# Kernel tuning notes

Hardware: AMD Instinct MI355X
Metric: run time of the kernel (lower is better)

## Reference

```python
import jax, jax.numpy as jnp
import numpy as np

N = 100000      # nodes
E = 1600000     # edges
R = 16          # relation types
IN_DIM = 32
HID = 64
NCLS = 8
B = 128         # graphs in batch


def setup_inputs() -> dict:
    key = jax.random.key(0)
    ks = jax.random.split(key, 16)
    h = jax.random.normal(ks[0], (N, IN_DIM), dtype=jnp.float32)
    src = jax.random.randint(ks[1], (E,), 0, N, dtype=jnp.int32)
    dst = jax.random.randint(ks[2], (E,), 0, N, dtype=jnp.int32)
    rel_types = jax.random.randint(ks[3], (E,), 0, R, dtype=jnp.int32)
    node2graph = jnp.sort(jax.random.randint(ks[4], (N,), 0, B, dtype=jnp.int32))
    s1 = 1.0 / np.sqrt(IN_DIM)
    s2 = 1.0 / np.sqrt(HID)
    W1 = jax.random.normal(ks[5], (R, IN_DIM, HID), dtype=jnp.float32) * s1
    Wloop1 = jax.random.normal(ks[6], (IN_DIM, HID), dtype=jnp.float32) * s1
    b1 = jnp.zeros((HID,), dtype=jnp.float32)
    W2 = jax.random.normal(ks[7], (R, HID, HID), dtype=jnp.float32) * s2
    Wloop2 = jax.random.normal(ks[8], (HID, HID), dtype=jnp.float32) * s2
    b2 = jnp.zeros((HID,), dtype=jnp.float32)
    Wc = jax.random.normal(ks[9], (HID, NCLS), dtype=jnp.float32) * s2
    bc = jnp.zeros((NCLS,), dtype=jnp.float32)
    return {"h": h, "src": src, "dst": dst, "rel_types": rel_types,
            "node2graph": node2graph, "W1": W1, "Wloop1": Wloop1, "b1": b1,
            "W2": W2, "Wloop2": Wloop2, "b2": b2, "Wc": Wc, "bc": bc}


def rel_graph_conv(h, src, dst, rel, W, Wloop, b):
    # h: [N, in], W: [R, in, out]. Transform all nodes by all relations once
    # (R small), then gather per-edge message indexed by (rel, src) and
    # scatter-sum to dst -- same math as DGL RelGraphConv (no edge norm),
    # with self-loop and bias (DGL defaults self_loop=True, bias=True).
    HR = jnp.einsum('ni,rio->rno', h, W)          # [R, N, out]
    msg = HR[rel, src]                            # [E, out]
    agg = jax.ops.segment_sum(msg, dst, num_segments=h.shape[0])
    return agg + h @ Wloop + b


def reference(h, src, dst, rel_types, node2graph,
              W1, Wloop1, b1, W2, Wloop2, b2, Wc, bc):
    h = h.astype(jnp.float32)
    h = jax.nn.relu(rel_graph_conv(h, src, dst, rel_types, W1, Wloop1, b1))
    h = jax.nn.relu(rel_graph_conv(h, src, dst, rel_types, W2, Wloop2, b2))
    # dgl.mean_nodes: per-graph mean pooling over nodes
    sums = jax.ops.segment_sum(h, node2graph, num_segments=B)      # [B, HID]
    cnts = jax.ops.segment_sum(jnp.ones((h.shape[0],), jnp.float32),
                               node2graph, num_segments=B)
    hg = sums / jnp.maximum(cnts, 1.0)[:, None]
    logits = hg @ Wc + bc
    return jax.nn.softmax(logits, axis=1)
```

## Files before the change

kernel.cpp:

```cpp
#include <hip/hip_runtime.h>
#include <hip/hip_bf16.h>


#define IN_DIM 32
#define HID 64
#define NREL 16
#define NCLS 8

__device__ __forceinline__ int rfl(int v) { return __builtin_amdgcn_readfirstlane(v); }


__global__ void hist_rel(const int* __restrict__ rel, int* __restrict__ hist, int E) {
  __shared__ int lh[NREL];
  int tid = threadIdx.x;
  if (tid < NREL) lh[tid] = 0;
  __syncthreads();
  for (int e = blockIdx.x * blockDim.x + tid; e < E; e += gridDim.x * blockDim.x)
    atomicAdd(&lh[rel[e]], 1);
  __syncthreads();
  if (tid < NREL && lh[tid] > 0) atomicAdd(&hist[tid], lh[tid]);
}

__global__ void scan16(const int* __restrict__ hist, int* __restrict__ offs,
                       int* __restrict__ fill) {
  if (threadIdx.x == 0) {
    int o = 0;
    for (int r = 0; r < NREL; ++r) {
      offs[r] = o;
      fill[r] = o;
      o += (hist[r] + 63) & ~63;
    }
    offs[NREL] = o;
  }
}

__global__ void fill_pad(int* __restrict__ ssrc, int* __restrict__ sdst, int Epad, int N) {
  int i = blockIdx.x * blockDim.x + threadIdx.x;
  if (i < Epad) { ssrc[i] = 0; sdst[i] = N; }
}

__global__ void scatter_rel(const int* __restrict__ rel, const int* __restrict__ src,
                            const int* __restrict__ dst, int* __restrict__ fill,
                            int* __restrict__ ssrc, int* __restrict__ sdst, int E) {
  __shared__ int lc[NREL];
  __shared__ int lbase[NREL];
  int tid = threadIdx.x;
  if (tid < NREL) lc[tid] = 0;
  __syncthreads();
  int e = blockIdx.x * blockDim.x + tid;
  int r = 0, lo = 0;
  bool valid = (e < E);
  if (valid) {
    r = rel[e];
    lo = atomicAdd(&lc[r], 1);
  }
  __syncthreads();
  if (tid < NREL && lc[tid] > 0) lbase[tid] = atomicAdd(&fill[tid], lc[tid]);
  __syncthreads();
  if (valid) {
    int p = lbase[r] + lo;
    ssrc[p] = src[e];
    sdst[p] = dst[e];
  }
}


template <int IN>
__global__ void edge_layer(const float* __restrict__ hin,
                           const int* __restrict__ ssrc,
                           const int* __restrict__ sdst,
                           const float* __restrict__ W,
                           const int* __restrict__ offs,
                           float* __restrict__ agg,
                           int maxchunks) {
  const int lane = threadIdx.x & 63;
  int wid = rfl((int)(blockIdx.x * (blockDim.x >> 6) + (threadIdx.x >> 6)));
  if (wid >= maxchunks) return;
  const int base = wid * 64;

  int r = 0;
#pragma unroll
  for (int k = 1; k < NREL; ++k) r += (base >= offs[k]) ? 1 : 0;

  const float* Wr = W + (size_t)r * (IN * HID);
  float w[IN];
#pragma unroll
  for (int i = 0; i < IN; ++i) w[i] = Wr[i * HID + lane];

  const int myd = sdst[base + lane];
  const int mys = ssrc[base + lane];

#pragma unroll 4
  for (int k = 0; k < 64; ++k) {
    const int d = __builtin_amdgcn_readlane(myd, k);
    const int s = __builtin_amdgcn_readlane(mys, k);
    const float4* __restrict__ row = (const float4*)(hin + (size_t)s * IN);
    float a0 = 0.f, a1 = 0.f, a2 = 0.f, a3 = 0.f;
#pragma unroll
    for (int i = 0; i < IN / 4; ++i) {
      float4 hv = row[i];
      a0 = fmaf(hv.x, w[4 * i + 0], a0);
      a1 = fmaf(hv.y, w[4 * i + 1], a1);
      a2 = fmaf(hv.z, w[4 * i + 2], a2);
      a3 = fmaf(hv.w, w[4 * i + 3], a3);
    }
    atomicAdd(&agg[(size_t)d * HID + lane], (a0 + a1) + (a2 + a3));
  }
}


__global__ void finalize1(const float* __restrict__ agg, const float* __restrict__ h,
                          const float* __restrict__ Wl, const float* __restrict__ b,
                          float* __restrict__ h1, int N) {
  const int lane = threadIdx.x & 63;
  int wid = rfl((int)(blockIdx.x * (blockDim.x >> 6) + (threadIdx.x >> 6)));
  int nw = gridDim.x * (blockDim.x >> 6);
  float wl[IN_DIM];
#pragma unroll
  for (int i = 0; i < IN_DIM; ++i) wl[i] = Wl[i * HID + lane];
  float bv = b[lane];
  for (int n = wid; n < N; n += nw) {
    const float4* __restrict__ row = (const float4*)(h + (size_t)n * IN_DIM);
    float a0 = 0.f, a1 = 0.f, a2 = 0.f, a3 = 0.f;
#pragma unroll
    for (int i = 0; i < IN_DIM / 4; ++i) {
      float4 hv = row[i];
      a0 = fmaf(hv.x, wl[4 * i + 0], a0);
      a1 = fmaf(hv.y, wl[4 * i + 1], a1);
      a2 = fmaf(hv.z, wl[4 * i + 2], a2);
      a3 = fmaf(hv.w, wl[4 * i + 3], a3);
    }
    float v = agg[(size_t)n * HID + lane] + (a0 + a1) + (a2 + a3) + bv;
    h1[(size_t)n * HID + lane] = fmaxf(v, 0.f);
  }
}

__global__ void finalize2_pool(const float* __restrict__ agg, const float* __restrict__ h1,
                               const float* __restrict__ Wl, const float* __restrict__ b,
                               const int* __restrict__ n2g,
                               float* __restrict__ pooled, float* __restrict__ cnt, int N) {
  const int lane = threadIdx.x & 63;
  int wid = rfl((int)(blockIdx.x * (blockDim.x >> 6) + (threadIdx.x >> 6)));
  int nw = gridDim.x * (blockDim.x >> 6);
  int per = (N + nw - 1) / nw;
  int n0 = wid * per;
  int n1 = min(N, n0 + per);
  if (n0 >= n1) return;

  float wl[HID];
#pragma unroll
  for (int i = 0; i < HID; ++i) wl[i] = Wl[i * HID + lane];
  float bv = b[lane];

  float psum = 0.f, pcnt = 0.f;
  int pg = -1;
  for (int n = n0; n < n1; ++n) {
    const float4* __restrict__ row = (const float4*)(h1 + (size_t)n * HID);
    float a0 = 0.f, a1 = 0.f, a2 = 0.f, a3 = 0.f;
#pragma unroll
    for (int i = 0; i < HID / 4; ++i) {
      float4 hv = row[i];
      a0 = fmaf(hv.x, wl[4 * i + 0], a0);
      a1 = fmaf(hv.y, wl[4 * i + 1], a1);
      a2 = fmaf(hv.z, wl[4 * i + 2], a2);
      a3 = fmaf(hv.w, wl[4 * i + 3], a3);
    }
    float v = agg[(size_t)n * HID + lane] + (a0 + a1) + (a2 + a3) + bv;
    v = fmaxf(v, 0.f);
    int g = rfl(n2g[n]);
    if (g != pg) {
      if (pg >= 0) {
        atomicAdd(&pooled[(size_t)pg * HID + lane], psum);
        if (lane == 0) atomicAdd(&cnt[pg], pcnt);
      }
      pg = g; psum = 0.f; pcnt = 0.f;
    }
    psum += v; pcnt += 1.f;
  }
  if (pg >= 0) {
    atomicAdd(&pooled[(size_t)pg * HID + lane], psum);
    if (lane == 0) atomicAdd(&cnt[pg], pcnt);
  }
}


__global__ void classifier(const float* __restrict__ pooled, const float* __restrict__ cnt,
                           const float* __restrict__ Wc, const float* __restrict__ bc,
                           float* __restrict__ out, int B) {
  int g = blockIdx.x * blockDim.x + threadIdx.x;
  if (g >= B) return;
  float c = fmaxf(cnt[g], 1.f);
  float lg[NCLS];
#pragma unroll
  for (int cc = 0; cc < NCLS; ++cc) lg[cc] = bc[cc];
  for (int k = 0; k < HID; ++k) {
    float hg = pooled[(size_t)g * HID + k] / c;
#pragma unroll
    for (int cc = 0; cc < NCLS; ++cc) lg[cc] = fmaf(hg, Wc[k * NCLS + cc], lg[cc]);
  }
  float m = lg[0];
#pragma unroll
  for (int cc = 1; cc < NCLS; ++cc) m = fmaxf(m, lg[cc]);
  float s = 0.f;
#pragma unroll
  for (int cc = 0; cc < NCLS; ++cc) { lg[cc] = __expf(lg[cc] - m); s += lg[cc]; }
  float inv = 1.f / s;
#pragma unroll
  for (int cc = 0; cc < NCLS; ++cc) out[(size_t)g * NCLS + cc] = lg[cc] * inv;
}


extern "C" void kernel_launch(void* const* d_in, const int* in_sizes, int n_in,
                              void* d_out, int out_size, void* d_ws, size_t ws_size,
                              hipStream_t stream) {
  const float* h   = (const float*)d_in[0];
  const int* src   = (const int*)d_in[1];
  const int* dst   = (const int*)d_in[2];
  const int* rel   = (const int*)d_in[3];
  const int* n2g   = (const int*)d_in[4];
  const float* W1  = (const float*)d_in[5];
  const float* Wl1 = (const float*)d_in[6];
  const float* b1  = (const float*)d_in[7];
  const float* W2  = (const float*)d_in[8];
  const float* Wl2 = (const float*)d_in[9];
  const float* b2  = (const float*)d_in[10];
  const float* Wc  = (const float*)d_in[11];
  const float* bc  = (const float*)d_in[12];

  const int N = in_sizes[0] / IN_DIM;
  const int E = in_sizes[1];
  const int B = out_size / NCLS;

  const int maxchunks = (E + 63) / 64 + NREL;
  const int Epad = maxchunks * 64;

  float* agg    = (float*)d_ws;
  float* h1     = agg + (size_t)(N + 1) * HID;
  int*   ssrc   = (int*)(h1 + (size_t)N * HID);
  int*   sdst   = ssrc + Epad;
  int*   hist   = sdst + Epad;
  int*   offs   = hist + NREL;
  int*   fill   = offs + NREL + 1;
  float* pooled = (float*)(fill + NREL);
  float* cnt    = pooled + (size_t)B * HID;

  hipMemsetAsync(hist, 0, NREL * sizeof(int), stream);
  hipMemsetAsync(pooled, 0, (size_t)(B * HID + B) * sizeof(float), stream);

  fill_pad<<<(Epad + 255) / 256, 256, 0, stream>>>(ssrc, sdst, Epad, N);
  hist_rel<<<1024, 256, 0, stream>>>(rel, hist, E);
  scan16<<<1, 64, 0, stream>>>(hist, offs, fill);
  scatter_rel<<<(E + 255) / 256, 256, 0, stream>>>(rel, src, dst, fill, ssrc, sdst, E);

  const int eblocks = (maxchunks + 3) / 4;

  hipMemsetAsync(agg, 0, (size_t)(N + 1) * HID * sizeof(float), stream);
  edge_layer<IN_DIM><<<eblocks, 256, 0, stream>>>(h, ssrc, sdst, W1, offs, agg, maxchunks);
  finalize1<<<2048, 256, 0, stream>>>(agg, h, Wl1, b1, h1, N);

  hipMemsetAsync(agg, 0, (size_t)(N + 1) * HID * sizeof(float), stream);
  edge_layer<HID><<<eblocks, 256, 0, stream>>>(h1, ssrc, sdst, W2, offs, agg, maxchunks);
  finalize2_pool<<<2048, 256, 0, stream>>>(agg, h1, Wl2, b2, n2g, pooled, cnt, N);

  classifier<<<(B + 127) / 128, 128, 0, stream>>>(pooled, cnt, Wc, bc, (float*)d_out, B);
}
```

Measured before the change: 980.0 us.

## Replace atomic scatter-add with per-edge message buffer and CSR gather by destination

Builds a destination CSR (histogram, three-stage scan, and an edge index into the relation-sorted order), then writes per-edge messages to a dense buffer and has each node gather its incoming messages. The self-loop, bias, ReLU and pooling are fused into the gather. This removes the float atomics on agg and its memsets. In exchange it writes and rereads a roughly 400 MB message buffer per layer and adds several preprocessing kernels. The new path runs only when the workspace is large enough, otherwise the old path is kept.

```diff
diff --git a/kernel.cpp b/kernel.cpp
--- a/kernel.cpp
+++ b/kernel.cpp
@@ -6,8 +6,10 @@
 #define HID 64
 #define NREL 16
 #define NCLS 8
+#define CHUNK 2048
 
 __device__ __forceinline__ int rfl(int v) { return __builtin_amdgcn_readfirstlane(v); }
+__device__ __forceinline__ int rl(int v, int l) { return __builtin_amdgcn_readlane(v, l); }
 
 
 __global__ void hist_rel(const int* __restrict__ rel, int* __restrict__ hist, int E) {
@@ -21,18 +23,241 @@
   if (tid < NREL && lh[tid] > 0) atomicAdd(&hist[tid], lh[tid]);
 }
 
+__global__ void hist_dst_k(const int* __restrict__ dst, int* __restrict__ histd, int E) {
+  for (int e = blockIdx.x * blockDim.x + threadIdx.x; e < E; e += gridDim.x * blockDim.x)
+    atomicAdd(&histd[dst[e]], 1);
+}
+
 __global__ void scan16(const int* __restrict__ hist, int* __restrict__ offs,
-                       int* __restrict__ fill) {
+                       int* __restrict__ fillrel) {
   if (threadIdx.x == 0) {
     int o = 0;
     for (int r = 0; r < NREL; ++r) {
       offs[r] = o;
-      fill[r] = o;
+      fillrel[r] = o;
       o += (hist[r] + 63) & ~63;
     }
     offs[NREL] = o;
   }
 }
+
+__global__ void pad_gaps(const int* __restrict__ hist, const int* __restrict__ offs,
+                         int* __restrict__ ssrc, int Epad) {
+  int r = blockIdx.x;
+  int lo = (r < NREL) ? offs[r] + hist[r] : offs[NREL];
+  int hi = (r < NREL) ? offs[r + 1] : Epad;
+  for (int i = lo + threadIdx.x; i < hi; i += blockDim.x) ssrc[i] = 0;
+}
+
+
+__global__ void scan1_k(const int* __restrict__ histd, int* __restrict__ csum, int N) {
+  __shared__ int red[256];
+  int t = threadIdx.x;
+  int base = blockIdx.x * CHUNK + t * 8;
+  int s = 0;
+#pragma unroll
+  for (int i = 0; i < 8; ++i) { int idx = base + i; s += (idx < N) ? histd[idx] : 0; }
+  red[t] = s; __syncthreads();
+  for (int off = 128; off > 0; off >>= 1) {
+    if (t < off) red[t] += red[t + off];
+    __syncthreads();
+  }
+  if (t == 0) csum[blockIdx.x] = red[0];
+}
+
+__global__ void scan2_k(const int* __restrict__ csum, int* __restrict__ cbase,
+                        int* __restrict__ rowptr, int nchunks, int N) {
+  if (threadIdx.x == 0) {
+    int run = 0;
+    for (int c = 0; c < nchunks; ++c) { cbase[c] = run; run += csum[c]; }
+    rowptr[N] = run;
+  }
+}
+
+__global__ void scan3_k(const int* __restrict__ histd, const int* __restrict__ cbase,
+                        int* __restrict__ rowptr, int* __restrict__ filldst, int N) {
+  __shared__ int ts[256];
+  int t = threadIdx.x;
+  int base = blockIdx.x * CHUNK + t * 8;
+  int v[8]; int s = 0;
+#pragma unroll
+  for (int i = 0; i < 8; ++i) { int idx = base + i; int x = (idx < N) ? histd[idx] : 0; v[i] = x; s += x; }
+  ts[t] = s; __syncthreads();
+  int x = s;
+  for (int off = 1; off < 256; off <<= 1) {
+    int y = (t >= off) ? ts[t - off] : 0;
+    __syncthreads();
+    x += y; ts[t] = x;
+    __syncthreads();
+  }
+  int run = cbase[blockIdx.x] + x - s;
+#pragma unroll
+  for (int i = 0; i < 8; ++i) {
+    int idx = base + i;
+    if (idx < N) { rowptr[idx] = run; filldst[idx] = run; run += v[i]; }
+  }
+}
+
+
+__global__ void scatter_rel2(const int* __restrict__ rel, const int* __restrict__ src,
+                             const int* __restrict__ dst, int* __restrict__ fillrel,
+                             int* __restrict__ filldst, int* __restrict__ ssrc,
+                             int* __restrict__ eidx, int E) {
+  __shared__ int lc[NREL];
+  __shared__ int lbase[NREL];
+  int tid = threadIdx.x;
+  if (tid < NREL) lc[tid] = 0;
+  __syncthreads();
+  int e = blockIdx.x * blockDim.x + tid;
+  int r = 0, lo = 0;
+  bool valid = (e < E);
+  if (valid) { r = rel[e]; lo = atomicAdd(&lc[r], 1); }
+  __syncthreads();
+  if (tid < NREL && lc[tid] > 0) lbase[tid] = atomicAdd(&fillrel[tid], lc[tid]);
+  __syncthreads();
+  if (valid) {
+    int p = lbase[r] + lo;
+    ssrc[p] = src[e];
+    int q = atomicAdd(&filldst[dst[e]], 1);
+    eidx[q] = p;
+  }
+}
+
+
+template <int IN>
+__global__ void edge_msg(const float* __restrict__ hin, const int* __restrict__ ssrc,
+                         const float* __restrict__ W, const int* __restrict__ offs,
+                         float* __restrict__ msg, int maxchunks) {
+  const int lane = threadIdx.x & 63;
+  int wid = rfl((int)(blockIdx.x * (blockDim.x >> 6) + (threadIdx.x >> 6)));
+  if (wid >= maxchunks) return;
+  const int base = wid * 64;
+
+  int r = 0;
+#pragma unroll
+  for (int k = 1; k < NREL; ++k) r += (base >= offs[k]) ? 1 : 0;
+
+  const float* Wr = W + (size_t)r * (IN * HID);
+  float w[IN];
+#pragma unroll
+  for (int i = 0; i < IN; ++i) w[i] = Wr[i * HID + lane];
+
+  const int mys = ssrc[base + lane];
+
+#pragma unroll 4
+  for (int k = 0; k < 64; ++k) {
+    const int s = rl(mys, k);
+    const float4* __restrict__ row = (const float4*)(hin + (size_t)s * IN);
+    float a0 = 0.f, a1 = 0.f, a2 = 0.f, a3 = 0.f;
+#pragma unroll
+    for (int i = 0; i < IN / 4; ++i) {
+      float4 hv = row[i];
+      a0 = fmaf(hv.x, w[4 * i + 0], a0);
+      a1 = fmaf(hv.y, w[4 * i + 1], a1);
+      a2 = fmaf(hv.z, w[4 * i + 2], a2);
+      a3 = fmaf(hv.w, w[4 * i + 3], a3);
+    }
+    msg[(size_t)(base + k) * HID + lane] = (a0 + a1) + (a2 + a3);
+  }
+}
+
+
+template <int IN, bool POOL>
+__global__ void gather_fin(const float* __restrict__ msg, const int* __restrict__ eidx,
+                           const int* __restrict__ rowptr, const float* __restrict__ hprev,
+                           const float* __restrict__ Wl, const float* __restrict__ b,
+                           const int* __restrict__ n2g, float* __restrict__ out,
+                           float* __restrict__ pooled, float* __restrict__ cnt, int N) {
+  const int lane = threadIdx.x & 63;
+  int wid = rfl((int)(blockIdx.x * (blockDim.x >> 6) + (threadIdx.x >> 6)));
+  int nw = gridDim.x * (blockDim.x >> 6);
+  int per = (N + nw - 1) / nw;
+  int n0 = wid * per, n1 = min(N, n0 + per);
+  if (n0 >= n1) return;
+
+  float wl[IN];
+#pragma unroll
+  for (int i = 0; i < IN; ++i) wl[i] = Wl[i * HID + lane];
+  float bv = b[lane];
+
+  float psum = 0.f, pcnt = 0.f;
+  int pg = -1;
+  for (int n = n0; n < n1; ++n) {
+    int j0 = rowptr[n], j1 = rowptr[n + 1];
+    float a0 = 0.f, a1 = 0.f, a2 = 0.f, a3 = 0.f;
+    int j = j0;
+    while (j < j1) {
+      int c = min(j1 - j, 64);
+      int vidx = (lane < c) ? eidx[j + lane] : 0;
+      int k = 0;
+      for (; k + 3 < c; k += 4) {
+        int i0 = rl(vidx, k), i1 = rl(vidx, k + 1), i2 = rl(vidx, k + 2), i3 = rl(vidx, k + 3);
+        a0 += msg[(size_t)i0 * HID + lane];
+        a1 += msg[(size_t)i1 * HID + lane];
+        a2 += msg[(size_t)i2 * HID + lane];
+        a3 += msg[(size_t)i3 * HID + lane];
+      }
+      for (; k < c; ++k) a0 += msg[(size_t)rl(vidx, k) * HID + lane];
+      j += c;
+    }
+    const float4* __restrict__ row = (const float4*)(hprev + (size_t)n * IN);
+    float s0 = 0.f, s1 = 0.f, s2 = 0.f, s3 = 0.f;
+#pragma unroll
+    for (int i = 0; i < IN / 4; ++i) {
+      float4 hv = row[i];
+      s0 = fmaf(hv.x, wl[4 * i + 0], s0);
+      s1 = fmaf(hv.y, wl[4 * i + 1], s1);
+      s2 = fmaf(hv.z, wl[4 * i + 2], s2);
+      s3 = fmaf(hv.w, wl[4 * i + 3], s3);
+    }
+    float v = (a0 + a1) + (a2 + a3) + (s0 + s1) + (s2 + s3) + bv;
+    v = fmaxf(v, 0.f);
+    if (POOL) {
+      int g = rfl(n2g[n]);
+      if (g != pg) {
+        if (pg >= 0) {
+          atomicAdd(&pooled[(size_t)pg * HID + lane], psum);
+          if (lane == 0) atomicAdd(&cnt[pg], pcnt);
+        }
+        pg = g; psum = 0.f; pcnt = 0.f;
+      }
+      psum += v; pcnt += 1.f;
+    } else {
+      out[(size_t)n * HID + lane] = v;
+    }
+  }
+  if (POOL && pg >= 0) {
+    atomicAdd(&pooled[(size_t)pg * HID + lane], psum);
+    if (lane == 0) atomicAdd(&cnt[pg], pcnt);
+  }
+}
+
+
+__global__ void classifier(const float* __restrict__ pooled, const float* __restrict__ cnt,
+                           const float* __restrict__ Wc, const float* __restrict__ bc,
+                           float* __restrict__ out, int B) {
+  int g = blockIdx.x * blockDim.x + threadIdx.x;
+  if (g >= B) return;
+  float c = fmaxf(cnt[g], 1.f);
+  float lg[NCLS];
+#pragma unroll
+  for (int cc = 0; cc < NCLS; ++cc) lg[cc] = bc[cc];
+  for (int k = 0; k < HID; ++k) {
+    float hg = pooled[(size_t)g * HID + k] / c;
+#pragma unroll
+    for (int cc = 0; cc < NCLS; ++cc) lg[cc] = fmaf(hg, Wc[k * NCLS + cc], lg[cc]);
+  }
+  float m = lg[0];
+#pragma unroll
+  for (int cc = 1; cc < NCLS; ++cc) m = fmaxf(m, lg[cc]);
+  float s = 0.f;
+#pragma unroll
+  for (int cc = 0; cc < NCLS; ++cc) { lg[cc] = __expf(lg[cc] - m); s += lg[cc]; }
+  float inv = 1.f / s;
+#pragma unroll
+  for (int cc = 0; cc < NCLS; ++cc) out[(size_t)g * NCLS + cc] = lg[cc] * inv;
+}
+
 
 __global__ void fill_pad(int* __restrict__ ssrc, int* __restrict__ sdst, int Epad, int N) {
   int i = blockIdx.x * blockDim.x + threadIdx.x;
@@ -50,50 +275,35 @@
   int e = blockIdx.x * blockDim.x + tid;
   int r = 0, lo = 0;
   bool valid = (e < E);
-  if (valid) {
-    r = rel[e];
-    lo = atomicAdd(&lc[r], 1);
-  }
+  if (valid) { r = rel[e]; lo = atomicAdd(&lc[r], 1); }
   __syncthreads();
   if (tid < NREL && lc[tid] > 0) lbase[tid] = atomicAdd(&fill[tid], lc[tid]);
   __syncthreads();
-  if (valid) {
-    int p = lbase[r] + lo;
-    ssrc[p] = src[e];
-    sdst[p] = dst[e];
-  }
-}
-
+  if (valid) { int p = lbase[r] + lo; ssrc[p] = src[e]; sdst[p] = dst[e]; }
+}
 
 template <int IN>
-__global__ void edge_layer(const float* __restrict__ hin,
-                           const int* __restrict__ ssrc,
-                           const int* __restrict__ sdst,
-                           const float* __restrict__ W,
-                           const int* __restrict__ offs,
-                           float* __restrict__ agg,
+__global__ void edge_layer(const float* __restrict__ hin, const int* __restrict__ ssrc,
+                           const int* __restrict__ sdst, const float* __restrict__ W,
+                           const int* __restrict__ offs, float* __restrict__ agg,
                            int maxchunks) {
   const int lane = threadIdx.x & 63;
   int wid = rfl((int)(blockIdx.x * (blockDim.x >> 6) + (threadIdx.x >> 6)));
   if (wid >= maxchunks) return;
   const int base = wid * 64;
-
   int r = 0;
 #pragma unroll
   for (int k = 1; k < NREL; ++k) r += (base >= offs[k]) ? 1 : 0;
-
   const float* Wr = W + (size_t)r * (IN * HID);
   float w[IN];
 #pragma unroll
   for (int i = 0; i < IN; ++i) w[i] = Wr[i * HID + lane];
-
   const int myd = sdst[base + lane];
   const int mys = ssrc[base + lane];
-
 #pragma unroll 4
   for (int k = 0; k < 64; ++k) {
-    const int d = __builtin_amdgcn_readlane(myd, k);
-    const int s = __builtin_amdgcn_readlane(mys, k);
+    const int d = rl(myd, k);
+    const int s = rl(mys, k);
     const float4* __restrict__ row = (const float4*)(hin + (size_t)s * IN);
     float a0 = 0.f, a1 = 0.f, a2 = 0.f, a3 = 0.f;
 #pragma unroll
@@ -107,7 +317,6 @@
     atomicAdd(&agg[(size_t)d * HID + lane], (a0 + a1) + (a2 + a3));
   }
 }
-
 
 __global__ void finalize1(const float* __restrict__ agg, const float* __restrict__ h,
                           const float* __restrict__ Wl, const float* __restrict__ b,
@@ -143,15 +352,12 @@
   int wid = rfl((int)(blockIdx.x * (blockDim.x >> 6) + (threadIdx.x >> 6)));
   int nw = gridDim.x * (blockDim.x >> 6);
   int per = (N + nw - 1) / nw;
-  int n0 = wid * per;
-  int n1 = min(N, n0 + per);
+  int n0 = wid * per, n1 = min(N, n0 + per);
   if (n0 >= n1) return;
-
   float wl[HID];
 #pragma unroll
   for (int i = 0; i < HID; ++i) wl[i] = Wl[i * HID + lane];
   float bv = b[lane];
-
   float psum = 0.f, pcnt = 0.f;
   int pg = -1;
   for (int n = n0; n < n1; ++n) {
@@ -181,32 +387,6 @@
     atomicAdd(&pooled[(size_t)pg * HID + lane], psum);
     if (lane == 0) atomicAdd(&cnt[pg], pcnt);
   }
-}
-
-
-__global__ void classifier(const float* __restrict__ pooled, const float* __restrict__ cnt,
-                           const float* __restrict__ Wc, const float* __restrict__ bc,
-                           float* __restrict__ out, int B) {
-  int g = blockIdx.x * blockDim.x + threadIdx.x;
-  if (g >= B) return;
-  float c = fmaxf(cnt[g], 1.f);
-  float lg[NCLS];
-#pragma unroll
-  for (int cc = 0; cc < NCLS; ++cc) lg[cc] = bc[cc];
-  for (int k = 0; k < HID; ++k) {
-    float hg = pooled[(size_t)g * HID + k] / c;
-#pragma unroll
-    for (int cc = 0; cc < NCLS; ++cc) lg[cc] = fmaf(hg, Wc[k * NCLS + cc], lg[cc]);
-  }
-  float m = lg[0];
-#pragma unroll
-  for (int cc = 1; cc < NCLS; ++cc) m = fmaxf(m, lg[cc]);
-  float s = 0.f;
-#pragma unroll
-  for (int cc = 0; cc < NCLS; ++cc) { lg[cc] = __expf(lg[cc] - m); s += lg[cc]; }
-  float inv = 1.f / s;
-#pragma unroll
-  for (int cc = 0; cc < NCLS; ++cc) out[(size_t)g * NCLS + cc] = lg[cc] * inv;
 }
 
 
@@ -233,6 +413,51 @@
 
   const int maxchunks = (E + 63) / 64 + NREL;
   const int Epad = maxchunks * 64;
+  const int nchunks = (N + CHUNK - 1) / CHUNK;
+  const int eblocks = (maxchunks + 3) / 4;
+
+  size_t need_elems = (size_t)N * HID + (size_t)Epad * HID + (size_t)Epad * 2 +
+                      (size_t)(N + 1) + N + N + nchunks * 2 + 49 +
+                      (size_t)B * HID + B + 64;
+  if (ws_size >= need_elems * 4) {
+    float* h1     = (float*)d_ws;
+    float* msg    = h1 + (size_t)N * HID;
+    int*   ssrc   = (int*)(msg + (size_t)Epad * HID);
+    int*   eidx   = ssrc + Epad;
+    int*   rowptr = eidx + Epad;
+    int*   filldst= rowptr + (N + 1);
+    int*   histd  = filldst + N;
+    int*   csum   = histd + N;
+    int*   cbase  = csum + nchunks;
+    int*   hist   = cbase + nchunks;
+    int*   offs   = hist + NREL;
+    int*   fillrel= offs + NREL + 1;
+    float* pooled = (float*)(fillrel + NREL);
+    float* cnt    = pooled + (size_t)B * HID;
+
+    hipMemsetAsync(hist, 0, NREL * sizeof(int), stream);
+    hipMemsetAsync(histd, 0, (size_t)N * sizeof(int), stream);
+    hipMemsetAsync(pooled, 0, (size_t)(B * HID + B) * sizeof(float), stream);
+
+    hist_rel<<<1024, 256, 0, stream>>>(rel, hist, E);
+    hist_dst_k<<<1024, 256, 0, stream>>>(dst, histd, E);
+    scan16<<<1, 64, 0, stream>>>(hist, offs, fillrel);
+    scan1_k<<<nchunks, 256, 0, stream>>>(histd, csum, N);
+    scan2_k<<<1, 64, 0, stream>>>(csum, cbase, rowptr, nchunks, N);
+    scan3_k<<<nchunks, 256, 0, stream>>>(histd, cbase, rowptr, filldst, N);
+    pad_gaps<<<NREL + 1, 64, 0, stream>>>(hist, offs, ssrc, Epad);
+    scatter_rel2<<<(E + 255) / 256, 256, 0, stream>>>(rel, src, dst, fillrel, filldst,
+                                                      ssrc, eidx, E);
+
+    edge_msg<IN_DIM><<<eblocks, 256, 0, stream>>>(h, ssrc, W1, offs, msg, maxchunks);
+    gather_fin<IN_DIM, false><<<1024, 256, 0, stream>>>(msg, eidx, rowptr, h, Wl1, b1,
+                                                        nullptr, h1, nullptr, nullptr, N);
+    edge_msg<HID><<<eblocks, 256, 0, stream>>>(h1, ssrc, W2, offs, msg, maxchunks);
+    gather_fin<HID, true><<<1024, 256, 0, stream>>>(msg, eidx, rowptr, h1, Wl2, b2,
+                                                    n2g, nullptr, pooled, cnt, N);
+    classifier<<<(B + 127) / 128, 128, 0, stream>>>(pooled, cnt, Wc, bc, (float*)d_out, B);
+    return;
+  }
 
   float* agg    = (float*)d_ws;
   float* h1     = agg + (size_t)(N + 1) * HID;
@@ -246,21 +471,15 @@
 
   hipMemsetAsync(hist, 0, NREL * sizeof(int), stream);
   hipMemsetAsync(pooled, 0, (size_t)(B * HID + B) * sizeof(float), stream);
-
   fill_pad<<<(Epad + 255) / 256, 256, 0, stream>>>(ssrc, sdst, Epad, N);
   hist_rel<<<1024, 256, 0, stream>>>(rel, hist, E);
   scan16<<<1, 64, 0, stream>>>(hist, offs, fill);
   scatter_rel<<<(E + 255) / 256, 256, 0, stream>>>(rel, src, dst, fill, ssrc, sdst, E);
-
-  const int eblocks = (maxchunks + 3) / 4;
-
   hipMemsetAsync(agg, 0, (size_t)(N + 1) * HID * sizeof(float), stream);
   edge_layer<IN_DIM><<<eblocks, 256, 0, stream>>>(h, ssrc, sdst, W1, offs, agg, maxchunks);
   finalize1<<<2048, 256, 0, stream>>>(agg, h, Wl1, b1, h1, N);
-
   hipMemsetAsync(agg, 0, (size_t)(N + 1) * HID * sizeof(float), stream);
   edge_layer<HID><<<eblocks, 256, 0, stream>>>(h1, ssrc, sdst, W2, offs, agg, maxchunks);
   finalize2_pool<<<2048, 256, 0, stream>>>(agg, h1, Wl2, b2, n2g, pooled, cnt, N);
-
   classifier<<<(B + 127) / 128, 128, 0, stream>>>(pooled, cnt, Wc, bc, (float*)d_out, B);
 }
```

Result: no change. 980.7 us (+0.1%).

## Replace relation-sorted atomic scatter with dst-sorted CSR gather and LDS-staged weights

Applied to the files above, without the earlier changes.

Builds a CSR by destination (histogram, three-stage scan, atomic fill) with src and relation packed into one int per edge. Each wave then owns a range of destination nodes and accumulates messages in registers, so the global float atomics of the edge pass go away. Relation weights are staged in swizzled shared memory in groups of relations, with one pass per group. The cost is re-reading the adjacency for every group (2 passes for layer 1, 4 for layer 2), a serial ballot loop per edge, and a CSR build that itself uses atomics. The old path is kept as a fallback when the workspace is too small.

```diff
diff --git a/kernel.cpp b/kernel.cpp
--- a/kernel.cpp
+++ b/kernel.cpp
@@ -6,105 +6,131 @@
 #define HID 64
 #define NREL 16
 #define NCLS 8
+#define CHUNK 2048
 
 __device__ __forceinline__ int rfl(int v) { return __builtin_amdgcn_readfirstlane(v); }
-
-
-__global__ void hist_rel(const int* __restrict__ rel, int* __restrict__ hist, int E) {
-  __shared__ int lh[NREL];
-  int tid = threadIdx.x;
-  if (tid < NREL) lh[tid] = 0;
-  __syncthreads();
-  for (int e = blockIdx.x * blockDim.x + tid; e < E; e += gridDim.x * blockDim.x)
-    atomicAdd(&lh[rel[e]], 1);
-  __syncthreads();
-  if (tid < NREL && lh[tid] > 0) atomicAdd(&hist[tid], lh[tid]);
-}
-
-__global__ void scan16(const int* __restrict__ hist, int* __restrict__ offs,
-                       int* __restrict__ fill) {
+__device__ __forceinline__ int rl(int v, int l) { return __builtin_amdgcn_readlane(v, l); }
+
+
+__global__ void hist_dst_k(const int* __restrict__ dst, int* __restrict__ histd, int E) {
+  for (int e = blockIdx.x * blockDim.x + threadIdx.x; e < E; e += gridDim.x * blockDim.x)
+    atomicAdd(&histd[dst[e]], 1);
+}
+
+__global__ void scan1_k(const int* __restrict__ histd, int* __restrict__ csum, int N) {
+  __shared__ int red[256];
+  int t = threadIdx.x;
+  int base = blockIdx.x * CHUNK + t * 8;
+  int s = 0;
+#pragma unroll
+  for (int i = 0; i < 8; ++i) { int idx = base + i; s += (idx < N) ? histd[idx] : 0; }
+  red[t] = s; __syncthreads();
+  for (int off = 128; off > 0; off >>= 1) {
+    if (t < off) red[t] += red[t + off];
+    __syncthreads();
+  }
+  if (t == 0) csum[blockIdx.x] = red[0];
+}
+
+__global__ void scan2_k(const int* __restrict__ csum, int* __restrict__ cbase,
+                        int* __restrict__ rowptr, int nchunks, int N) {
   if (threadIdx.x == 0) {
-    int o = 0;
-    for (int r = 0; r < NREL; ++r) {
-      offs[r] = o;
-      fill[r] = o;
-      o += (hist[r] + 63) & ~63;
-    }
-    offs[NREL] = o;
-  }
-}
-
-__global__ void fill_pad(int* __restrict__ ssrc, int* __restrict__ sdst, int Epad, int N) {
-  int i = blockIdx.x * blockDim.x + threadIdx.x;
-  if (i < Epad) { ssrc[i] = 0; sdst[i] = N; }
-}
-
-__global__ void scatter_rel(const int* __restrict__ rel, const int* __restrict__ src,
-                            const int* __restrict__ dst, int* __restrict__ fill,
-                            int* __restrict__ ssrc, int* __restrict__ sdst, int E) {
-  __shared__ int lc[NREL];
-  __shared__ int lbase[NREL];
-  int tid = threadIdx.x;
-  if (tid < NREL) lc[tid] = 0;
-  __syncthreads();
-  int e = blockIdx.x * blockDim.x + tid;
-  int r = 0, lo = 0;
-  bool valid = (e < E);
-  if (valid) {
-    r = rel[e];
-    lo = atomicAdd(&lc[r], 1);
-  }
-  __syncthreads();
-  if (tid < NREL && lc[tid] > 0) lbase[tid] = atomicAdd(&fill[tid], lc[tid]);
-  __syncthreads();
-  if (valid) {
-    int p = lbase[r] + lo;
-    ssrc[p] = src[e];
-    sdst[p] = dst[e];
-  }
-}
-
-
-template <int IN>
-__global__ void edge_layer(const float* __restrict__ hin,
-                           const int* __restrict__ ssrc,
-                           const int* __restrict__ sdst,
-                           const float* __restrict__ W,
-                           const int* __restrict__ offs,
-                           float* __restrict__ agg,
-                           int maxchunks) {
+    int run = 0;
+    for (int c = 0; c < nchunks; ++c) { cbase[c] = run; run += csum[c]; }
+    rowptr[N] = run;
+  }
+}
+
+__global__ void scan3_k(const int* __restrict__ histd, const int* __restrict__ cbase,
+                        int* __restrict__ rowptr, int* __restrict__ filldst, int N) {
+  __shared__ int ts[256];
+  int t = threadIdx.x;
+  int base = blockIdx.x * CHUNK + t * 8;
+  int v[8]; int s = 0;
+#pragma unroll
+  for (int i = 0; i < 8; ++i) { int idx = base + i; int x = (idx < N) ? histd[idx] : 0; v[i] = x; s += x; }
+  ts[t] = s; __syncthreads();
+  int x = s;
+  for (int off = 1; off < 256; off <<= 1) {
+    int y = (t >= off) ? ts[t - off] : 0;
+    __syncthreads();
+    x += y; ts[t] = x;
+    __syncthreads();
+  }
+  int run = cbase[blockIdx.x] + x - s;
+#pragma unroll
+  for (int i = 0; i < 8; ++i) {
+    int idx = base + i;
+    if (idx < N) { rowptr[idx] = run; filldst[idx] = run; run += v[i]; }
+  }
+}
+
+__global__ void scatter_pack(const int* __restrict__ src, const int* __restrict__ dst,
+                             const int* __restrict__ rel, int* __restrict__ filldst,
+                             int* __restrict__ epack, int E) {
+  int e = blockIdx.x * blockDim.x + threadIdx.x;
+  if (e < E) {
+    int q = atomicAdd(&filldst[dst[e]], 1);
+    epack[q] = (src[e] << 4) | rel[e];
+  }
+}
+
+
+template <int K, int GSZ, bool FIRST>
+__global__ __launch_bounds__(512, 4)
+void edge_pass(const float* __restrict__ hin, const int* __restrict__ epack,
+               const int* __restrict__ rowptr, const float* __restrict__ W,
+               float* __restrict__ out, int N, int g) {
+  __shared__ float lw[GSZ * K * 64];
+  const float* __restrict__ Wg = W + (size_t)g * GSZ * K * 64;
+  for (int s = threadIdx.x; s < GSZ * K * 64; s += blockDim.x) {
+    int rloc = s / (K * 64);
+    int rem  = s - rloc * (K * 64);
+    int i = rem >> 6;
+    int o = rem & 63;
+    lw[rloc * (K * 64) + o * K + ((o & (K - 1)) ^ i)] = Wg[s];
+  }
+  __syncthreads();
+
   const int lane = threadIdx.x & 63;
-  int wid = rfl((int)(blockIdx.x * (blockDim.x >> 6) + (threadIdx.x >> 6)));
-  if (wid >= maxchunks) return;
-  const int base = wid * 64;
-
-  int r = 0;
-#pragma unroll
-  for (int k = 1; k < NREL; ++k) r += (base >= offs[k]) ? 1 : 0;
-
-  const float* Wr = W + (size_t)r * (IN * HID);
-  float w[IN];
-#pragma unroll
-  for (int i = 0; i < IN; ++i) w[i] = Wr[i * HID + lane];
-
-  const int myd = sdst[base + lane];
-  const int mys = ssrc[base + lane];
-
-#pragma unroll 4
-  for (int k = 0; k < 64; ++k) {
-    const int d = __builtin_amdgcn_readlane(myd, k);
-    const int s = __builtin_amdgcn_readlane(mys, k);
-    const float4* __restrict__ row = (const float4*)(hin + (size_t)s * IN);
-    float a0 = 0.f, a1 = 0.f, a2 = 0.f, a3 = 0.f;
-#pragma unroll
-    for (int i = 0; i < IN / 4; ++i) {
-      float4 hv = row[i];
-      a0 = fmaf(hv.x, w[4 * i + 0], a0);
-      a1 = fmaf(hv.y, w[4 * i + 1], a1);
-      a2 = fmaf(hv.z, w[4 * i + 2], a2);
-      a3 = fmaf(hv.w, w[4 * i + 3], a3);
-    }
-    atomicAdd(&agg[(size_t)d * HID + lane], (a0 + a1) + (a2 + a3));
+  const int nw  = gridDim.x * (blockDim.x >> 6);
+  const int wid = blockIdx.x * (blockDim.x >> 6) + (threadIdx.x >> 6);
+  const int per = (N + nw - 1) / nw;
+  const int n0 = wid * per, n1 = min(N, n0 + per);
+  const int fb0 = lane * K + (lane & (K - 1));
+  const int SH = (GSZ == 8) ? 3 : 2;
+
+  for (int n = n0; n < n1; ++n) {
+    const int j0 = rowptr[n], j1 = rowptr[n + 1];
+    float acc = 0.f;
+    bool any = false;
+    for (int j = j0; j < j1; j += 64) {
+      const int c = min(j1 - j, 64);
+      const int bv = (lane < c) ? epack[j + lane] : 0;
+      unsigned long long m = __ballot(lane < c && (((bv & 15) >> SH) == g));
+      any |= (m != 0ull);
+      while (m) {
+        const int k = (int)__builtin_ctzll(m);
+        m &= m - 1;
+        const int v = rl(bv, k);
+        const int s = v >> 4;
+        const int rloc = (v & 15) - g * GSZ;
+        const float4* __restrict__ row = (const float4*)(hin + (size_t)s * K);
+        const float* __restrict__ lwp = lw + rloc * (K * 64);
+        float a0 = 0.f, a1 = 0.f, a2 = 0.f, a3 = 0.f;
+#pragma unroll
+        for (int q = 0; q < K / 4; ++q) {
+          float4 hv = row[q];
+          a0 = fmaf(hv.x, lwp[fb0 ^ (4 * q + 0)], a0);
+          a1 = fmaf(hv.y, lwp[fb0 ^ (4 * q + 1)], a1);
+          a2 = fmaf(hv.z, lwp[fb0 ^ (4 * q + 2)], a2);
+          a3 = fmaf(hv.w, lwp[fb0 ^ (4 * q + 3)], a3);
+        }
+        acc += (a0 + a1) + (a2 + a3);
+      }
+    }
+    if (FIRST) out[(size_t)n * HID + lane] = acc;
+    else if (any) out[(size_t)n * HID + lane] += acc;
   }
 }
 
@@ -143,15 +169,12 @@
   int wid = rfl((int)(blockIdx.x * (blockDim.x >> 6) + (threadIdx.x >> 6)));
   int nw = gridDim.x * (blockDim.x >> 6);
   int per = (N + nw - 1) / nw;
-  int n0 = wid * per;
-  int n1 = min(N, n0 + per);
+  int n0 = wid * per, n1 = min(N, n0 + per);
   if (n0 >= n1) return;
-
   float wl[HID];
 #pragma unroll
   for (int i = 0; i < HID; ++i) wl[i] = Wl[i * HID + lane];
   float bv = b[lane];
-
   float psum = 0.f, pcnt = 0.f;
   int pg = -1;
   for (int n = n0; n < n1; ++n) {
@@ -207,6 +230,89 @@
   float inv = 1.f / s;
 #pragma unroll
   for (int cc = 0; cc < NCLS; ++cc) out[(size_t)g * NCLS + cc] = lg[cc] * inv;
+}
+
+
+__global__ void hist_rel(const int* __restrict__ rel, int* __restrict__ hist, int E) {
+  __shared__ int lh[NREL];
+  int tid = threadIdx.x;
+  if (tid < NREL) lh[tid] = 0;
+  __syncthreads();
+  for (int e = blockIdx.x * blockDim.x + tid; e < E; e += gridDim.x * blockDim.x)
+    atomicAdd(&lh[rel[e]], 1);
+  __syncthreads();
+  if (tid < NREL && lh[tid] > 0) atomicAdd(&hist[tid], lh[tid]);
+}
+
+__global__ void scan16(const int* __restrict__ hist, int* __restrict__ offs,
+                       int* __restrict__ fill) {
+  if (threadIdx.x == 0) {
+    int o = 0;
+    for (int r = 0; r < NREL; ++r) {
+      offs[r] = o; fill[r] = o;
+      o += (hist[r] + 63) & ~63;
+    }
+    offs[NREL] = o;
+  }
+}
+
+__global__ void fill_pad(int* __restrict__ ssrc, int* __restrict__ sdst, int Epad, int N) {
+  int i = blockIdx.x * blockDim.x + threadIdx.x;
+  if (i < Epad) { ssrc[i] = 0; sdst[i] = N; }
+}
+
+__global__ void scatter_rel(const int* __restrict__ rel, const int* __restrict__ src,
+                            const int* __restrict__ dst, int* __restrict__ fill,
+                            int* __restrict__ ssrc, int* __restrict__ sdst, int E) {
+  __shared__ int lc[NREL];
+  __shared__ int lbase[NREL];
+  int tid = threadIdx.x;
+  if (tid < NREL) lc[tid] = 0;
+  __syncthreads();
+  int e = blockIdx.x * blockDim.x + tid;
+  int r = 0, lo = 0;
+  bool valid = (e < E);
+  if (valid) { r = rel[e]; lo = atomicAdd(&lc[r], 1); }
+  __syncthreads();
+  if (tid < NREL && lc[tid] > 0) lbase[tid] = atomicAdd(&fill[tid], lc[tid]);
+  __syncthreads();
+  if (valid) { int p = lbase[r] + lo; ssrc[p] = src[e]; sdst[p] = dst[e]; }
+}
+
+template <int IN>
+__global__ void edge_layer(const float* __restrict__ hin, const int* __restrict__ ssrc,
+                           const int* __restrict__ sdst, const float* __restrict__ W,
+                           const int* __restrict__ offs, float* __restrict__ agg,
+                           int maxchunks) {
+  const int lane = threadIdx.x & 63;
+  int wid = rfl((int)(blockIdx.x * (blockDim.x >> 6) + (threadIdx.x >> 6)));
+  if (wid >= maxchunks) return;
+  const int base = wid * 64;
+  int r = 0;
+#pragma unroll
+  for (int k = 1; k < NREL; ++k) r += (base >= offs[k]) ? 1 : 0;
+  const float* Wr = W + (size_t)r * (IN * HID);
+  float w[IN];
+#pragma unroll
+  for (int i = 0; i < IN; ++i) w[i] = Wr[i * HID + lane];
+  const int myd = sdst[base + lane];
+  const int mys = ssrc[base + lane];
+#pragma unroll 4
+  for (int k = 0; k < 64; ++k) {
+    const int d = rl(myd, k);
+    const int s = rl(mys, k);
+    const float4* __restrict__ row = (const float4*)(hin + (size_t)s * IN);
+    float a0 = 0.f, a1 = 0.f, a2 = 0.f, a3 = 0.f;
+#pragma unroll
+    for (int i = 0; i < IN / 4; ++i) {
+      float4 hv = row[i];
+      a0 = fmaf(hv.x, w[4 * i + 0], a0);
+      a1 = fmaf(hv.y, w[4 * i + 1], a1);
+      a2 = fmaf(hv.z, w[4 * i + 2], a2);
+      a3 = fmaf(hv.w, w[4 * i + 3], a3);
+    }
+    atomicAdd(&agg[(size_t)d * HID + lane], (a0 + a1) + (a2 + a3));
+  }
 }
 
 
@@ -230,10 +336,48 @@
   const int N = in_sizes[0] / IN_DIM;
   const int E = in_sizes[1];
   const int B = out_size / NCLS;
+  const int nchunks = (N + CHUNK - 1) / CHUNK;
+
+  size_t need = (size_t)N * HID * 2 + (size_t)E + (size_t)(N + 1) + 2 * (size_t)N +
+                2 * (size_t)nchunks + (size_t)B * HID + B + 64;
+  if (ws_size >= need * 4) {
+    float* tmp    = (float*)d_ws;
+    float* h1     = tmp + (size_t)N * HID;
+    int*   epack  = (int*)(h1 + (size_t)N * HID);
+    int*   rowptr = epack + E;
+    int*   filldst= rowptr + (N + 1);
+    int*   histd  = filldst + N;
+    int*   csum   = histd + N;
+    int*   cbase  = csum + nchunks;
+    float* pooled = (float*)(cbase + nchunks);
+    float* cnt    = pooled + (size_t)B * HID;
+
+    hipMemsetAsync(histd, 0, (size_t)N * sizeof(int), stream);
+    hipMemsetAsync(pooled, 0, (size_t)(B * HID + B) * sizeof(float), stream);
+
+    hist_dst_k<<<1024, 256, 0, stream>>>(dst, histd, E);
+    scan1_k<<<nchunks, 256, 0, stream>>>(histd, csum, N);
+    scan2_k<<<1, 64, 0, stream>>>(csum, cbase, rowptr, nchunks, N);
+    scan3_k<<<nchunks, 256, 0, stream>>>(histd, cbase, rowptr, filldst, N);
+    scatter_pack<<<(E + 255) / 256, 256, 0, stream>>>(src, dst, rel, filldst, epack, E);
+
+    edge_pass<IN_DIM, 8, true ><<<512, 512, 0, stream>>>(h, epack, rowptr, W1, tmp, N, 0);
+    edge_pass<IN_DIM, 8, false><<<512, 512, 0, stream>>>(h, epack, rowptr, W1, tmp, N, 1);
+    finalize1<<<2048, 256, 0, stream>>>(tmp, h, Wl1, b1, h1, N);
+
+    edge_pass<HID, 4, true ><<<512, 512, 0, stream>>>(h1, epack, rowptr, W2, tmp, N, 0);
+    edge_pass<HID, 4, false><<<512, 512, 0, stream>>>(h1, epack, rowptr, W2, tmp, N, 1);
+    edge_pass<HID, 4, false><<<512, 512, 0, stream>>>(h1, epack, rowptr, W2, tmp, N, 2);
+    edge_pass<HID, 4, false><<<512, 512, 0, stream>>>(h1, epack, rowptr, W2, tmp, N, 3);
+    finalize2_pool<<<2048, 256, 0, stream>>>(tmp, h1, Wl2, b2, n2g, pooled, cnt, N);
+
+    classifier<<<(B + 127) / 128, 128, 0, stream>>>(pooled, cnt, Wc, bc, (float*)d_out, B);
+    return;
+  }
 
   const int maxchunks = (E + 63) / 64 + NREL;
   const int Epad = maxchunks * 64;
-
+  const int eblocks = (maxchunks + 3) / 4;
   float* agg    = (float*)d_ws;
   float* h1     = agg + (size_t)(N + 1) * HID;
   int*   ssrc   = (int*)(h1 + (size_t)N * HID);
@@ -246,21 +390,15 @@
 
   hipMemsetAsync(hist, 0, NREL * sizeof(int), stream);
   hipMemsetAsync(pooled, 0, (size_t)(B * HID + B) * sizeof(float), stream);
-
   fill_pad<<<(Epad + 255) / 256, 256, 0, stream>>>(ssrc, sdst, Epad, N);
   hist_rel<<<1024, 256, 0, stream>>>(rel, hist, E);
   scan16<<<1, 64, 0, stream>>>(hist, offs, fill);
   scatter_rel<<<(E + 255) / 256, 256, 0, stream>>>(rel, src, dst, fill, ssrc, sdst, E);
-
-  const int eblocks = (maxchunks + 3) / 4;
-
   hipMemsetAsync(agg, 0, (size_t)(N + 1) * HID * sizeof(float), stream);
   edge_layer<IN_DIM><<<eblocks, 256, 0, stream>>>(h, ssrc, sdst, W1, offs, agg, maxchunks);
   finalize1<<<2048, 256, 0, stream>>>(agg, h, Wl1, b1, h1, N);
-
   hipMemsetAsync(agg, 0, (size_t)(N + 1) * HID * sizeof(float), stream);
   edge_layer<HID><<<eblocks, 256, 0, stream>>>(h1, ssrc, sdst, W2, offs, agg, maxchunks);
   finalize2_pool<<<2048, 256, 0, stream>>>(agg, h1, Wl2, b2, n2g, pooled, cnt, N);
-
   classifier<<<(B + 127) / 128, 128, 0, stream>>>(pooled, cnt, Wc, bc, (float*)d_out, B);
 }
```

Measured after the change: 1.492 ms. +52.3%, slower.
